# Kernel optimization log

Hardware: AMD Instinct MI355X
Metric: run time of the kernel (lower is better)

Reference implementation:

```python
import jax, jax.numpy as jnp
import numpy as np


def setup_inputs() -> dict:
    key = jax.random.key(0)
    k1, k2, k3 = jax.random.split(key, 3)
    N, M, H = 32768, 4096, 768
    fact = jax.random.normal(k1, (N, H), dtype=jnp.float32)
    elements_p = jax.random.normal(k2, (M, H), dtype=jnp.float32)
    # kaiming_uniform with a=sqrt(5) on [H,H]: bound = sqrt(6/((1+5)*H)) = 1/sqrt(H)
    bound = 1.0 / np.sqrt(H)
    weights = jax.random.uniform(k3, (H, H), dtype=jnp.float32, minval=-bound, maxval=bound)
    return {"fact": fact, "elements_p": elements_p, "weights": weights}


def reference(fact, elements_p, weights):
    # fact: [N,H], elements_p: [M,H], weights: [H,H]
    fact_Q = jnp.max(fact, axis=0, keepdims=True)                 # [1,H]
    f2e = (fact_Q @ weights) @ elements_p.T                        # [1,M]
    f2e = jax.nn.softmax(f2e, axis=-1)
    elements_p_ = jnp.sum(elements_p * f2e.T, axis=0, keepdims=True)  # [1,H]
    e2f = (fact @ weights) @ elements_p_.T                         # [N,1]
    e2f = jax.nn.softmax(e2f, axis=0)
    fact_ = jnp.sum(fact * e2f, axis=0, keepdims=True)             # [1,H]
    return (fact_, elements_p_)
```

## Files before the change

kernel.cpp:

```cpp
#include <hip/hip_runtime.h>
#include <math.h>


#define H 768
#define H4 192
#define PSTRIDE 772
#define ACC_OFF 4

__global__ __launch_bounds__(192) void k_colmax(const float4* __restrict__ x4,
                                                float4* __restrict__ pmax4, int N) {
  const int t = threadIdx.x;
  const int rpb = (N + gridDim.x - 1) / gridDim.x;
  const int n0 = blockIdx.x * rpb;
  const int n1 = min(N, n0 + rpb);
  float4 m = make_float4(-INFINITY, -INFINITY, -INFINITY, -INFINITY);
#pragma unroll 8
  for (int n = n0; n < n1; ++n) {
    float4 x = x4[(size_t)n * H4 + t];
    m.x = fmaxf(m.x, x.x); m.y = fmaxf(m.y, x.y);
    m.z = fmaxf(m.z, x.z); m.w = fmaxf(m.w, x.w);
  }
  pmax4[(size_t)blockIdx.x * H4 + t] = m;
}

__global__ __launch_bounds__(192) void k_q(const float4* __restrict__ W4,
                                           const float* __restrict__ pmax,
                                           float* __restrict__ q, int B) {
  const int tid = threadIdx.x;
  const int k0 = blockIdx.x * 16;
  __shared__ float sA[12][16];
  __shared__ float fQl[16];
  {
    const int col = tid & 15;
    const int grp = tid >> 4;
    float m = -INFINITY;
    for (int p = grp; p < B; p += 12) m = fmaxf(m, pmax[(size_t)p * H + k0 + col]);
    sA[grp][col] = m;
    __syncthreads();
    if (tid < 16) {
      float mm = sA[0][tid];
#pragma unroll
      for (int g = 1; g < 12; ++g) mm = fmaxf(mm, sA[g][tid]);
      fQl[tid] = mm;
    }
    __syncthreads();
  }
  float4 acc = make_float4(0.f, 0.f, 0.f, 0.f);
#pragma unroll 4
  for (int kk = 0; kk < 16; ++kk) {
    const float f = fQl[kk];
    const float4 w = W4[(size_t)(k0 + kk) * H4 + tid];
    acc.x = fmaf(f, w.x, acc.x);
    acc.y = fmaf(f, w.y, acc.y);
    acc.z = fmaf(f, w.z, acc.z);
    acc.w = fmaf(f, w.w, acc.w);
  }
  atomicAdd(&q[4 * tid + 0], acc.x);
  atomicAdd(&q[4 * tid + 1], acc.y);
  atomicAdd(&q[4 * tid + 2], acc.z);
  atomicAdd(&q[4 * tid + 3], acc.w);
}

template <int NW>
__global__ __launch_bounds__(NW * 64) void k_pass(const float4* __restrict__ X4,
                                                  const float* __restrict__ wvec,
                                                  float* __restrict__ part, int R,
                                                  unsigned int* __restrict__ cnt,
                                                  float* __restrict__ outA,
                                                  float* __restrict__ outB) {
  const int lane = threadIdx.x & 63;
  const int wv = threadIdx.x >> 6;
  const int NB = gridDim.x;
  __shared__ float sm[NW], sl[NW];
  __shared__ float4 sacc[NW][H4];

  {
    const int gw = blockIdx.x * NW + wv;
    const int nw = NB * NW;
    float4 wr[3];
#pragma unroll
    for (int j = 0; j < 3; ++j) wr[j] = ((const float4*)wvec)[lane + 64 * j];
    const int rpw = (R + nw - 1) / nw;
    const int r0 = gw * rpw;
    const int r1 = min(R, r0 + rpw);
    float mrun = -INFINITY, l = 0.f;
    float4 acc[3];
#pragma unroll
    for (int j = 0; j < 3; ++j) acc[j] = make_float4(0.f, 0.f, 0.f, 0.f);
    for (int r = r0; r < r1; ++r) {
      const float4* row = X4 + (size_t)r * H4;
      float4 x[3];
      float s = 0.f;
#pragma unroll
      for (int j = 0; j < 3; ++j) {
        x[j] = row[lane + 64 * j];
        s = fmaf(x[j].x, wr[j].x, s);
        s = fmaf(x[j].y, wr[j].y, s);
        s = fmaf(x[j].z, wr[j].z, s);
        s = fmaf(x[j].w, wr[j].w, s);
      }
#pragma unroll
      for (int o = 32; o; o >>= 1) s += __shfl_xor(s, o, 64);
      const float mn = fmaxf(mrun, s);
      const float esc = __expf(mrun - mn);
      const float p = __expf(s - mn);
      l = fmaf(l, esc, p);
#pragma unroll
      for (int j = 0; j < 3; ++j) {
        acc[j].x = fmaf(acc[j].x, esc, p * x[j].x);
        acc[j].y = fmaf(acc[j].y, esc, p * x[j].y);
        acc[j].z = fmaf(acc[j].z, esc, p * x[j].z);
        acc[j].w = fmaf(acc[j].w, esc, p * x[j].w);
      }
      mrun = mn;
    }
    if (lane == 0) { sm[wv] = mrun; sl[wv] = l; }
#pragma unroll
    for (int j = 0; j < 3; ++j) sacc[wv][lane + 64 * j] = acc[j];
    __syncthreads();
    if (wv == 0) {
      float gm = -INFINITY;
#pragma unroll
      for (int w2 = 0; w2 < NW; ++w2) gm = fmaxf(gm, sm[w2]);
      float fa[NW];
      float L = 0.f;
#pragma unroll
      for (int w2 = 0; w2 < NW; ++w2) {
        fa[w2] = (sl[w2] > 0.f) ? __expf(sm[w2] - gm) : 0.f;
        L = fmaf(fa[w2], sl[w2], L);
      }
      float* pb = part + (size_t)blockIdx.x * PSTRIDE;
#pragma unroll
      for (int j = 0; j < 3; ++j) {
        float4 a = make_float4(0.f, 0.f, 0.f, 0.f);
#pragma unroll
        for (int w2 = 0; w2 < NW; ++w2) {
          const float4 t = sacc[w2][lane + 64 * j];
          a.x = fmaf(fa[w2], t.x, a.x);
          a.y = fmaf(fa[w2], t.y, a.y);
          a.z = fmaf(fa[w2], t.z, a.z);
          a.w = fmaf(fa[w2], t.w, a.w);
        }
        *(float4*)(pb + ACC_OFF + 4 * (lane + 64 * j)) = a;
      }
      if (lane == 0) { pb[0] = gm; pb[1] = L; }
    }
  }

  __syncthreads();
  __shared__ unsigned int s_last;
  if (threadIdx.x == 0) {
    __threadfence();
    s_last = atomicAdd(cnt, 1u);
  }
  __syncthreads();
  if (s_last != (unsigned)(NB - 1)) return;
  __threadfence();

  {
    __shared__ float sred[NW];
    const float* P = part;
    float gm = -INFINITY;
    for (int b = threadIdx.x; b < NB; b += NW * 64) gm = fmaxf(gm, P[(size_t)b * PSTRIDE]);
#pragma unroll
    for (int o = 32; o; o >>= 1) gm = fmaxf(gm, __shfl_xor(gm, o, 64));
    if (lane == 0) sred[wv] = gm;
    __syncthreads();
    gm = sred[0];
#pragma unroll
    for (int w2 = 1; w2 < NW; ++w2) gm = fmaxf(gm, sred[w2]);
    __syncthreads();
    float L = 0.f;
    for (int b = threadIdx.x; b < NB; b += NW * 64) {
      const float m = P[(size_t)b * PSTRIDE];
      const float lb = P[(size_t)b * PSTRIDE + 1];
      L = fmaf((lb > 0.f) ? __expf(m - gm) : 0.f, lb, L);
    }
#pragma unroll
    for (int o = 32; o; o >>= 1) L += __shfl_xor(L, o, 64);
    if (lane == 0) sred[wv] = L;
    float4 a[3];
#pragma unroll
    for (int j = 0; j < 3; ++j) a[j] = make_float4(0.f, 0.f, 0.f, 0.f);
    for (int b = wv; b < NB; b += NW) {
      const float m = P[(size_t)b * PSTRIDE];
      const float lb = P[(size_t)b * PSTRIDE + 1];
      const float e = (lb > 0.f) ? __expf(m - gm) : 0.f;
      const float4* pa = (const float4*)(P + (size_t)b * PSTRIDE + ACC_OFF);
#pragma unroll
      for (int j = 0; j < 3; ++j) {
        const float4 t = pa[lane + 64 * j];
        a[j].x = fmaf(e, t.x, a[j].x);
        a[j].y = fmaf(e, t.y, a[j].y);
        a[j].z = fmaf(e, t.z, a[j].z);
        a[j].w = fmaf(e, t.w, a[j].w);
      }
    }
#pragma unroll
    for (int j = 0; j < 3; ++j) sacc[wv][lane + 64 * j] = a[j];
    __syncthreads();
    if (threadIdx.x < H4) {
      float4 s = sacc[0][threadIdx.x];
#pragma unroll
      for (int w2 = 1; w2 < NW; ++w2) {
        const float4 t = sacc[w2][threadIdx.x];
        s.x += t.x; s.y += t.y; s.z += t.z; s.w += t.w;
      }
      float Lt = sred[0];
#pragma unroll
      for (int w2 = 1; w2 < NW; ++w2) Lt += sred[w2];
      const float inv = 1.f / Lt;
      const float4 r = make_float4(s.x * inv, s.y * inv, s.z * inv, s.w * inv);
      ((float4*)outA)[threadIdx.x] = r;
      if (outB) ((float4*)outB)[threadIdx.x] = r;
    }
  }
}

__global__ __launch_bounds__(256) void k_v(const float4* __restrict__ W4,
                                           const float* __restrict__ ep_,
                                           float* __restrict__ v) {
  const int lane = threadIdx.x & 63;
  const int i = blockIdx.x * 4 + (threadIdx.x >> 6);
  float s = 0.f;
#pragma unroll
  for (int j = 0; j < 3; ++j) {
    const float4 w = W4[(size_t)i * H4 + lane + 64 * j];
    const float4 e = ((const float4*)ep_)[lane + 64 * j];
    s = fmaf(w.x, e.x, s);
    s = fmaf(w.y, e.y, s);
    s = fmaf(w.z, e.z, s);
    s = fmaf(w.w, e.w, s);
  }
#pragma unroll
  for (int o = 32; o; o >>= 1) s += __shfl_xor(s, o, 64);
  if (lane == 0) v[i] = s;
}

extern "C" void kernel_launch(void* const* d_in, const int* in_sizes, int n_in,
                              void* d_out, int out_size, void* d_ws, size_t ws_size,
                              hipStream_t stream) {
  const float* fact = (const float*)d_in[0];
  const float* ep   = (const float*)d_in[1];
  const float* W    = (const float*)d_in[2];
  float* out = (float*)d_out;
  const int N = in_sizes[0] / H;
  const int M = in_sizes[1] / H;

  const int B1 = 256;
  const int BM = 128;
  const int BN = 256;

  float* wsf  = (float*)d_ws;
  unsigned int* cnt2 = (unsigned int*)d_ws;
  unsigned int* cnt3 = (unsigned int*)d_ws + 1;
  float* q    = wsf + 4;
  float* epws = wsf + 772;
  float* v    = wsf + 1540;
  float* pmax = wsf + 2308;
  float* pm   = pmax + (size_t)B1 * H;
  float* pn   = pm + (size_t)BM * PSTRIDE;

  hipMemsetAsync(d_ws, 0, 3088, stream);
  k_colmax<<<B1, 192, 0, stream>>>((const float4*)fact, (float4*)pmax, N);
  k_q<<<48, 192, 0, stream>>>((const float4*)W, pmax, q, B1);
  k_pass<8><<<BM, 512, 0, stream>>>((const float4*)ep, q, pm, M, cnt2, epws, out + H);
  k_v<<<192, 256, 0, stream>>>((const float4*)W, epws, v);
  k_pass<8><<<BN, 512, 0, stream>>>((const float4*)fact, v, pn, N, cnt3, out, nullptr);
}
```

Baseline: 241.0 us.

## Fuse q projection, elements pass and v projection into one kernel; drop memset

Removes the memset by having the column-max kernel zero the counters, and fuses the q computation (global max reduce plus fQ@W) into the start of every elements-pass block. The last-arriving block then computes v = W·ep_ directly, which removes the separate k_q and k_v launches and their atomics. This cuts five launches plus a memset down to three kernels. The cost is that each of the 48 elements blocks redundantly reads all of W and the partial maxima. The elements pass also runs on fewer blocks, and the v matvec runs on a single block.

```diff
diff --git a/kernel.cpp b/kernel.cpp
--- a/kernel.cpp
+++ b/kernel.cpp
@@ -6,89 +6,102 @@
 #define H4 192
 #define PSTRIDE 772
 #define ACC_OFF 4
+#define B1 256
+#define B2 48
+#define B3 256
+
+__device__ __forceinline__ float wave_max(float x) {
+#pragma unroll
+  for (int o = 32; o; o >>= 1) x = fmaxf(x, __shfl_xor(x, o, 64));
+  return x;
+}
+__device__ __forceinline__ float wave_sum(float x) {
+#pragma unroll
+  for (int o = 32; o; o >>= 1) x += __shfl_xor(x, o, 64);
+  return x;
+}
+__device__ __forceinline__ float4 f4max(float4 a, float4 b) {
+  return make_float4(fmaxf(a.x, b.x), fmaxf(a.y, b.y), fmaxf(a.z, b.z), fmaxf(a.w, b.w));
+}
 
 __global__ __launch_bounds__(192) void k_colmax(const float4* __restrict__ x4,
-                                                float4* __restrict__ pmax4, int N) {
+                                                float4* __restrict__ pmax4, int N,
+                                                unsigned int* __restrict__ cnts) {
+  if (blockIdx.x == 0 && threadIdx.x < 2) cnts[threadIdx.x] = 0u;
   const int t = threadIdx.x;
-  const int rpb = (N + gridDim.x - 1) / gridDim.x;
+  const int rpb = (N + B1 - 1) / B1;
   const int n0 = blockIdx.x * rpb;
   const int n1 = min(N, n0 + rpb);
   float4 m = make_float4(-INFINITY, -INFINITY, -INFINITY, -INFINITY);
 #pragma unroll 8
-  for (int n = n0; n < n1; ++n) {
-    float4 x = x4[(size_t)n * H4 + t];
-    m.x = fmaxf(m.x, x.x); m.y = fmaxf(m.y, x.y);
-    m.z = fmaxf(m.z, x.z); m.w = fmaxf(m.w, x.w);
-  }
+  for (int n = n0; n < n1; ++n) m = f4max(m, x4[(size_t)n * H4 + t]);
   pmax4[(size_t)blockIdx.x * H4 + t] = m;
 }
 
-__global__ __launch_bounds__(192) void k_q(const float4* __restrict__ W4,
-                                           const float* __restrict__ pmax,
-                                           float* __restrict__ q, int B) {
+__global__ __launch_bounds__(512) void k_ep(const float4* __restrict__ ep4,
+                                            const float4* __restrict__ W4,
+                                            const float4* __restrict__ pmax4,
+                                            float* __restrict__ part, int M,
+                                            unsigned int* __restrict__ cnt,
+                                            float* __restrict__ out_ep,
+                                            float* __restrict__ v) {
   const int tid = threadIdx.x;
-  const int k0 = blockIdx.x * 16;
-  __shared__ float sA[12][16];
-  __shared__ float fQl[16];
+  const int lane = tid & 63;
+  const int wv = tid >> 6;
+  __shared__ float4 sacc[8][H4];
+  __shared__ float4 fq4[H4];
+  __shared__ float4 qarr4[H4];
+  __shared__ float sred[16];
+  __shared__ float se[B2];
+  __shared__ unsigned int s_last;
+
+  if (tid < 2 * H4) {
+    const int g = tid / H4, c = tid % H4;
+    float4 m = make_float4(-INFINITY, -INFINITY, -INFINITY, -INFINITY);
+#pragma unroll 8
+    for (int p = g; p < B1; p += 2) m = f4max(m, pmax4[(size_t)p * H4 + c]);
+    ((float4*)sacc)[g * H4 + c] = m;
+  }
+  __syncthreads();
+  if (tid < H4) fq4[tid] = f4max(((float4*)sacc)[tid], ((float4*)sacc)[H4 + tid]);
+  __syncthreads();
+  if (tid < 2 * H4) {
+    const int g = tid / H4, c = tid % H4;
+    const float* fq = (const float*)fq4;
+    float4 a = make_float4(0.f, 0.f, 0.f, 0.f);
+#pragma unroll 4
+    for (int k = g * 384; k < g * 384 + 384; ++k) {
+      const float f = fq[k];
+      const float4 w = W4[(size_t)k * H4 + c];
+      a.x = fmaf(f, w.x, a.x);
+      a.y = fmaf(f, w.y, a.y);
+      a.z = fmaf(f, w.z, a.z);
+      a.w = fmaf(f, w.w, a.w);
+    }
+    ((float4*)sacc)[g * H4 + c] = a;
+  }
+  __syncthreads();
+  if (tid < H4) {
+    const float4 a = ((float4*)sacc)[tid], b = ((float4*)sacc)[H4 + tid];
+    qarr4[tid] = make_float4(a.x + b.x, a.y + b.y, a.z + b.z, a.w + b.w);
+  }
+  __syncthreads();
+
   {
-    const int col = tid & 15;
-    const int grp = tid >> 4;
-    float m = -INFINITY;
-    for (int p = grp; p < B; p += 12) m = fmaxf(m, pmax[(size_t)p * H + k0 + col]);
-    sA[grp][col] = m;
-    __syncthreads();
-    if (tid < 16) {
-      float mm = sA[0][tid];
-#pragma unroll
-      for (int g = 1; g < 12; ++g) mm = fmaxf(mm, sA[g][tid]);
-      fQl[tid] = mm;
-    }
-    __syncthreads();
-  }
-  float4 acc = make_float4(0.f, 0.f, 0.f, 0.f);
-#pragma unroll 4
-  for (int kk = 0; kk < 16; ++kk) {
-    const float f = fQl[kk];
-    const float4 w = W4[(size_t)(k0 + kk) * H4 + tid];
-    acc.x = fmaf(f, w.x, acc.x);
-    acc.y = fmaf(f, w.y, acc.y);
-    acc.z = fmaf(f, w.z, acc.z);
-    acc.w = fmaf(f, w.w, acc.w);
-  }
-  atomicAdd(&q[4 * tid + 0], acc.x);
-  atomicAdd(&q[4 * tid + 1], acc.y);
-  atomicAdd(&q[4 * tid + 2], acc.z);
-  atomicAdd(&q[4 * tid + 3], acc.w);
-}
-
-template <int NW>
-__global__ __launch_bounds__(NW * 64) void k_pass(const float4* __restrict__ X4,
-                                                  const float* __restrict__ wvec,
-                                                  float* __restrict__ part, int R,
-                                                  unsigned int* __restrict__ cnt,
-                                                  float* __restrict__ outA,
-                                                  float* __restrict__ outB) {
-  const int lane = threadIdx.x & 63;
-  const int wv = threadIdx.x >> 6;
-  const int NB = gridDim.x;
-  __shared__ float sm[NW], sl[NW];
-  __shared__ float4 sacc[NW][H4];
-
-  {
-    const int gw = blockIdx.x * NW + wv;
-    const int nw = NB * NW;
     float4 wr[3];
 #pragma unroll
-    for (int j = 0; j < 3; ++j) wr[j] = ((const float4*)wvec)[lane + 64 * j];
-    const int rpw = (R + nw - 1) / nw;
+    for (int j = 0; j < 3; ++j) wr[j] = qarr4[lane + 64 * j];
+    const int nw = B2 * 8;
+    const int gw = blockIdx.x * 8 + wv;
+    const int rpw = (M + nw - 1) / nw;
     const int r0 = gw * rpw;
-    const int r1 = min(R, r0 + rpw);
+    const int r1 = min(M, r0 + rpw);
     float mrun = -INFINITY, l = 0.f;
     float4 acc[3];
 #pragma unroll
     for (int j = 0; j < 3; ++j) acc[j] = make_float4(0.f, 0.f, 0.f, 0.f);
     for (int r = r0; r < r1; ++r) {
-      const float4* row = X4 + (size_t)r * H4;
+      const float4* row = ep4 + (size_t)r * H4;
       float4 x[3];
       float s = 0.f;
 #pragma unroll
@@ -99,8 +112,7 @@
         s = fmaf(x[j].z, wr[j].z, s);
         s = fmaf(x[j].w, wr[j].w, s);
       }
-#pragma unroll
-      for (int o = 32; o; o >>= 1) s += __shfl_xor(s, o, 64);
+      s = wave_sum(s);
       const float mn = fmaxf(mrun, s);
       const float esc = __expf(mrun - mn);
       const float p = __expf(s - mn);
@@ -114,27 +126,28 @@
       }
       mrun = mn;
     }
-    if (lane == 0) { sm[wv] = mrun; sl[wv] = l; }
+    if (lane == 0) { sred[wv] = mrun; sred[8 + wv] = l; }
 #pragma unroll
     for (int j = 0; j < 3; ++j) sacc[wv][lane + 64 * j] = acc[j];
     __syncthreads();
     if (wv == 0) {
       float gm = -INFINITY;
 #pragma unroll
-      for (int w2 = 0; w2 < NW; ++w2) gm = fmaxf(gm, sm[w2]);
-      float fa[NW];
+      for (int w2 = 0; w2 < 8; ++w2) gm = fmaxf(gm, sred[w2]);
+      float fa[8];
       float L = 0.f;
 #pragma unroll
-      for (int w2 = 0; w2 < NW; ++w2) {
-        fa[w2] = (sl[w2] > 0.f) ? __expf(sm[w2] - gm) : 0.f;
-        L = fmaf(fa[w2], sl[w2], L);
+      for (int w2 = 0; w2 < 8; ++w2) {
+        const float lw = sred[8 + w2];
+        fa[w2] = (lw > 0.f) ? __expf(sred[w2] - gm) : 0.f;
+        L = fmaf(fa[w2], lw, L);
       }
       float* pb = part + (size_t)blockIdx.x * PSTRIDE;
 #pragma unroll
       for (int j = 0; j < 3; ++j) {
         float4 a = make_float4(0.f, 0.f, 0.f, 0.f);
 #pragma unroll
-        for (int w2 = 0; w2 < NW; ++w2) {
+        for (int w2 = 0; w2 < 8; ++w2) {
           const float4 t = sacc[w2][lane + 64 * j];
           a.x = fmaf(fa[w2], t.x, a.x);
           a.y = fmaf(fa[w2], t.y, a.y);
@@ -148,41 +161,205 @@
   }
 
   __syncthreads();
-  __shared__ unsigned int s_last;
-  if (threadIdx.x == 0) {
+  if (tid == 0) {
     __threadfence();
     s_last = atomicAdd(cnt, 1u);
   }
   __syncthreads();
-  if (s_last != (unsigned)(NB - 1)) return;
+  if (s_last != (unsigned)(B2 - 1)) return;
   __threadfence();
 
   {
-    __shared__ float sred[NW];
     const float* P = part;
     float gm = -INFINITY;
-    for (int b = threadIdx.x; b < NB; b += NW * 64) gm = fmaxf(gm, P[(size_t)b * PSTRIDE]);
-#pragma unroll
-    for (int o = 32; o; o >>= 1) gm = fmaxf(gm, __shfl_xor(gm, o, 64));
+    for (int b = tid; b < B2; b += 512) gm = fmaxf(gm, P[(size_t)b * PSTRIDE]);
+    gm = wave_max(gm);
     if (lane == 0) sred[wv] = gm;
     __syncthreads();
     gm = sred[0];
 #pragma unroll
-    for (int w2 = 1; w2 < NW; ++w2) gm = fmaxf(gm, sred[w2]);
-    __syncthreads();
+    for (int w2 = 1; w2 < 8; ++w2) gm = fmaxf(gm, sred[w2]);
     float L = 0.f;
-    for (int b = threadIdx.x; b < NB; b += NW * 64) {
+    for (int b = tid; b < B2; b += 512) {
+      const float m = P[(size_t)b * PSTRIDE];
+      const float lb = P[(size_t)b * PSTRIDE + 1];
+      const float e = (lb > 0.f) ? __expf(m - gm) : 0.f;
+      se[b] = e;
+      L = fmaf(e, lb, L);
+    }
+    L = wave_sum(L);
+    if (lane == 0) sred[8 + wv] = L;
+    __syncthreads();
+    float Lt = sred[8];
+#pragma unroll
+    for (int w2 = 1; w2 < 8; ++w2) Lt += sred[8 + w2];
+    if (tid < H4) {
+      float4 a = make_float4(0.f, 0.f, 0.f, 0.f);
+#pragma unroll 4
+      for (int b = 0; b < B2; ++b) {
+        const float e = se[b];
+        const float4 t = *(const float4*)(P + (size_t)b * PSTRIDE + ACC_OFF + 4 * tid);
+        a.x = fmaf(e, t.x, a.x);
+        a.y = fmaf(e, t.y, a.y);
+        a.z = fmaf(e, t.z, a.z);
+        a.w = fmaf(e, t.w, a.w);
+      }
+      const float inv = 1.f / Lt;
+      const float4 r = make_float4(a.x * inv, a.y * inv, a.z * inv, a.w * inv);
+      ((float4*)out_ep)[tid] = r;
+      fq4[tid] = r;
+    }
+    __syncthreads();
+    float4 er[3];
+#pragma unroll
+    for (int j = 0; j < 3; ++j) er[j] = fq4[lane + 64 * j];
+    for (int i0 = wv * 96; i0 < wv * 96 + 96; i0 += 4) {
+      float s0 = 0.f, s1 = 0.f, s2 = 0.f, s3 = 0.f;
+#pragma unroll
+      for (int j = 0; j < 3; ++j) {
+        const float4 e = er[j];
+        const float4 w0 = W4[(size_t)(i0 + 0) * H4 + lane + 64 * j];
+        const float4 w1 = W4[(size_t)(i0 + 1) * H4 + lane + 64 * j];
+        const float4 w2 = W4[(size_t)(i0 + 2) * H4 + lane + 64 * j];
+        const float4 w3 = W4[(size_t)(i0 + 3) * H4 + lane + 64 * j];
+        s0 = fmaf(w0.x, e.x, s0); s0 = fmaf(w0.y, e.y, s0);
+        s0 = fmaf(w0.z, e.z, s0); s0 = fmaf(w0.w, e.w, s0);
+        s1 = fmaf(w1.x, e.x, s1); s1 = fmaf(w1.y, e.y, s1);
+        s1 = fmaf(w1.z, e.z, s1); s1 = fmaf(w1.w, e.w, s1);
+        s2 = fmaf(w2.x, e.x, s2); s2 = fmaf(w2.y, e.y, s2);
+        s2 = fmaf(w2.z, e.z, s2); s2 = fmaf(w2.w, e.w, s2);
+        s3 = fmaf(w3.x, e.x, s3); s3 = fmaf(w3.y, e.y, s3);
+        s3 = fmaf(w3.z, e.z, s3); s3 = fmaf(w3.w, e.w, s3);
+      }
+#pragma unroll
+      for (int o = 32; o; o >>= 1) {
+        s0 += __shfl_xor(s0, o, 64);
+        s1 += __shfl_xor(s1, o, 64);
+        s2 += __shfl_xor(s2, o, 64);
+        s3 += __shfl_xor(s3, o, 64);
+      }
+      if (lane == 0) ((float4*)v)[i0 >> 2] = make_float4(s0, s1, s2, s3);
+    }
+  }
+}
+
+__global__ __launch_bounds__(512) void k_fact(const float4* __restrict__ X4,
+                                              const float* __restrict__ wvec,
+                                              float* __restrict__ part, int R,
+                                              unsigned int* __restrict__ cnt,
+                                              float* __restrict__ outp) {
+  const int tid = threadIdx.x;
+  const int lane = tid & 63;
+  const int wv = tid >> 6;
+  __shared__ float sm[8], sl[8];
+  __shared__ float4 sacc[8][H4];
+  __shared__ unsigned int s_last;
+
+  {
+    float4 wr[3];
+#pragma unroll
+    for (int j = 0; j < 3; ++j) wr[j] = ((const float4*)wvec)[lane + 64 * j];
+    const int nw = B3 * 8;
+    const int gw = blockIdx.x * 8 + wv;
+    const int rpw = (R + nw - 1) / nw;
+    const int r0 = gw * rpw;
+    const int r1 = min(R, r0 + rpw);
+    float mrun = -INFINITY, l = 0.f;
+    float4 acc[3];
+#pragma unroll
+    for (int j = 0; j < 3; ++j) acc[j] = make_float4(0.f, 0.f, 0.f, 0.f);
+    for (int r = r0; r < r1; ++r) {
+      const float4* row = X4 + (size_t)r * H4;
+      float4 x[3];
+      float s = 0.f;
+#pragma unroll
+      for (int j = 0; j < 3; ++j) {
+        x[j] = row[lane + 64 * j];
+        s = fmaf(x[j].x, wr[j].x, s);
+        s = fmaf(x[j].y, wr[j].y, s);
+        s = fmaf(x[j].z, wr[j].z, s);
+        s = fmaf(x[j].w, wr[j].w, s);
+      }
+      s = wave_sum(s);
+      const float mn = fmaxf(mrun, s);
+      const float esc = __expf(mrun - mn);
+      const float p = __expf(s - mn);
+      l = fmaf(l, esc, p);
+#pragma unroll
+      for (int j = 0; j < 3; ++j) {
+        acc[j].x = fmaf(acc[j].x, esc, p * x[j].x);
+        acc[j].y = fmaf(acc[j].y, esc, p * x[j].y);
+        acc[j].z = fmaf(acc[j].z, esc, p * x[j].z);
+        acc[j].w = fmaf(acc[j].w, esc, p * x[j].w);
+      }
+      mrun = mn;
+    }
+    if (lane == 0) { sm[wv] = mrun; sl[wv] = l; }
+#pragma unroll
+    for (int j = 0; j < 3; ++j) sacc[wv][lane + 64 * j] = acc[j];
+    __syncthreads();
+    if (wv == 0) {
+      float gm = -INFINITY;
+#pragma unroll
+      for (int w2 = 0; w2 < 8; ++w2) gm = fmaxf(gm, sm[w2]);
+      float fa[8];
+      float L = 0.f;
+#pragma unroll
+      for (int w2 = 0; w2 < 8; ++w2) {
+        fa[w2] = (sl[w2] > 0.f) ? __expf(sm[w2] - gm) : 0.f;
+        L = fmaf(fa[w2], sl[w2], L);
+      }
+      float* pb = part + (size_t)blockIdx.x * PSTRIDE;
+#pragma unroll
+      for (int j = 0; j < 3; ++j) {
+        float4 a = make_float4(0.f, 0.f, 0.f, 0.f);
+#pragma unroll
+        for (int w2 = 0; w2 < 8; ++w2) {
+          const float4 t = sacc[w2][lane + 64 * j];
+          a.x = fmaf(fa[w2], t.x, a.x);
+          a.y = fmaf(fa[w2], t.y, a.y);
+          a.z = fmaf(fa[w2], t.z, a.z);
+          a.w = fmaf(fa[w2], t.w, a.w);
+        }
+        *(float4*)(pb + ACC_OFF + 4 * (lane + 64 * j)) = a;
+      }
+      if (lane == 0) { pb[0] = gm; pb[1] = L; }
+    }
+  }
+
+  __syncthreads();
+  if (tid == 0) {
+    __threadfence();
+    s_last = atomicAdd(cnt, 1u);
+  }
+  __syncthreads();
+  if (s_last != (unsigned)(B3 - 1)) return;
+  __threadfence();
+
+  {
+    __shared__ float sred[16];
+    const float* P = part;
+    float gm = -INFINITY;
+    for (int b = tid; b < B3; b += 512) gm = fmaxf(gm, P[(size_t)b * PSTRIDE]);
+    gm = wave_max(gm);
+    if (lane == 0) sred[wv] = gm;
+    __syncthreads();
+    gm = sred[0];
+#pragma unroll
+    for (int w2 = 1; w2 < 8; ++w2) gm = fmaxf(gm, sred[w2]);
+    __syncthreads();
+    float L = 0.f;
+    for (int b = tid; b < B3; b += 512) {
       const float m = P[(size_t)b * PSTRIDE];
       const float lb = P[(size_t)b * PSTRIDE + 1];
       L = fmaf((lb > 0.f) ? __expf(m - gm) : 0.f, lb, L);
     }
-#pragma unroll
-    for (int o = 32; o; o >>= 1) L += __shfl_xor(L, o, 64);
-    if (lane == 0) sred[wv] = L;
+    L = wave_sum(L);
+    if (lane == 0) sred[8 + wv] = L;
     float4 a[3];
 #pragma unroll
     for (int j = 0; j < 3; ++j) a[j] = make_float4(0.f, 0.f, 0.f, 0.f);
-    for (int b = wv; b < NB; b += NW) {
+    for (int b = wv; b < B3; b += 8) {
       const float m = P[(size_t)b * PSTRIDE];
       const float lb = P[(size_t)b * PSTRIDE + 1];
       const float e = (lb > 0.f) ? __expf(m - gm) : 0.f;
@@ -199,72 +376,40 @@
 #pragma unroll
     for (int j = 0; j < 3; ++j) sacc[wv][lane + 64 * j] = a[j];
     __syncthreads();
-    if (threadIdx.x < H4) {
-      float4 s = sacc[0][threadIdx.x];
-#pragma unroll
-      for (int w2 = 1; w2 < NW; ++w2) {
-        const float4 t = sacc[w2][threadIdx.x];
+    if (tid < H4) {
+      float4 s = sacc[0][tid];
+#pragma unroll
+      for (int w2 = 1; w2 < 8; ++w2) {
+        const float4 t = sacc[w2][tid];
         s.x += t.x; s.y += t.y; s.z += t.z; s.w += t.w;
       }
-      float Lt = sred[0];
-#pragma unroll
-      for (int w2 = 1; w2 < NW; ++w2) Lt += sred[w2];
+      float Lt = sred[8];
+#pragma unroll
+      for (int w2 = 1; w2 < 8; ++w2) Lt += sred[8 + w2];
       const float inv = 1.f / Lt;
-      const float4 r = make_float4(s.x * inv, s.y * inv, s.z * inv, s.w * inv);
-      ((float4*)outA)[threadIdx.x] = r;
-      if (outB) ((float4*)outB)[threadIdx.x] = r;
-    }
-  }
-}
-
-__global__ __launch_bounds__(256) void k_v(const float4* __restrict__ W4,
-                                           const float* __restrict__ ep_,
-                                           float* __restrict__ v) {
-  const int lane = threadIdx.x & 63;
-  const int i = blockIdx.x * 4 + (threadIdx.x >> 6);
-  float s = 0.f;
-#pragma unroll
-  for (int j = 0; j < 3; ++j) {
-    const float4 w = W4[(size_t)i * H4 + lane + 64 * j];
-    const float4 e = ((const float4*)ep_)[lane + 64 * j];
-    s = fmaf(w.x, e.x, s);
-    s = fmaf(w.y, e.y, s);
-    s = fmaf(w.z, e.z, s);
-    s = fmaf(w.w, e.w, s);
-  }
-#pragma unroll
-  for (int o = 32; o; o >>= 1) s += __shfl_xor(s, o, 64);
-  if (lane == 0) v[i] = s;
+      ((float4*)outp)[tid] = make_float4(s.x * inv, s.y * inv, s.z * inv, s.w * inv);
+    }
+  }
 }
 
 extern "C" void kernel_launch(void* const* d_in, const int* in_sizes, int n_in,
                               void* d_out, int out_size, void* d_ws, size_t ws_size,
                               hipStream_t stream) {
-  const float* fact = (const float*)d_in[0];
-  const float* ep   = (const float*)d_in[1];
-  const float* W    = (const float*)d_in[2];
+  const float4* fact4 = (const float4*)d_in[0];
+  const float4* ep4   = (const float4*)d_in[1];
+  const float4* W4    = (const float4*)d_in[2];
   float* out = (float*)d_out;
   const int N = in_sizes[0] / H;
   const int M = in_sizes[1] / H;
 
-  const int B1 = 256;
-  const int BM = 128;
-  const int BN = 256;
-
-  float* wsf  = (float*)d_ws;
-  unsigned int* cnt2 = (unsigned int*)d_ws;
-  unsigned int* cnt3 = (unsigned int*)d_ws + 1;
-  float* q    = wsf + 4;
-  float* epws = wsf + 772;
-  float* v    = wsf + 1540;
-  float* pmax = wsf + 2308;
-  float* pm   = pmax + (size_t)B1 * H;
-  float* pn   = pm + (size_t)BM * PSTRIDE;
-
-  hipMemsetAsync(d_ws, 0, 3088, stream);
-  k_colmax<<<B1, 192, 0, stream>>>((const float4*)fact, (float4*)pmax, N);
-  k_q<<<48, 192, 0, stream>>>((const float4*)W, pmax, q, B1);
-  k_pass<8><<<BM, 512, 0, stream>>>((const float4*)ep, q, pm, M, cnt2, epws, out + H);
-  k_v<<<192, 256, 0, stream>>>((const float4*)W, epws, v);
-  k_pass<8><<<BN, 512, 0, stream>>>((const float4*)fact, v, pn, N, cnt3, out, nullptr);
-}
+  float* wsf = (float*)d_ws;
+  unsigned int* cnts = (unsigned int*)d_ws;
+  float* v = wsf + 4;
+  float4* pmax4 = (float4*)(wsf + 4 + H);
+  float* pm = wsf + 4 + H + B1 * H;
+  float* pn = pm + (size_t)B2 * PSTRIDE;
+
+  k_colmax<<<B1, 192, 0, stream>>>(fact4, pmax4, N, cnts);
+  k_ep<<<B2, 512, 0, stream>>>(ep4, W4, pmax4, pm, M, cnts + 0, out + H, v);
+  k_fact<<<B3, 512, 0, stream>>>(fact4, v, pn, N, cnts + 1, out);
+}
```

Measured after the change: 307.0 us. 27.4% more time.

## Fuse W·ep_ matvec into last block of ep pass and drop memset launch

Applied to the files above, without the earlier changes.

Removes the hipMemsetAsync by zeroing counters and q inside block 0 of the colmax kernel. Folds the separate k_v matvec into the last-arriving block of the elements pass, which computes v from the combined ep_ held in LDS. Also raises the elements-pass grid from 128 to 256 blocks. Together these cut two launches, but the W·ep_ product (768x768) now runs serially on a single block after the grid-wide combine. The memset-to-colmax move also relies on kernel ordering: k_q's atomics must not start before block 0 has zeroed q.

```diff
diff --git a/kernel.cpp b/kernel.cpp
--- a/kernel.cpp
+++ b/kernel.cpp
@@ -6,20 +6,186 @@
 #define H4 192
 #define PSTRIDE 772
 #define ACC_OFF 4
+#define B1 256
+#define BQ 48
+#define B2 256
+#define B3 256
+
+__device__ __forceinline__ float wave_max(float x) {
+#pragma unroll
+  for (int o = 32; o; o >>= 1) x = fmaxf(x, __shfl_xor(x, o, 64));
+  return x;
+}
+__device__ __forceinline__ float wave_sum(float x) {
+#pragma unroll
+  for (int o = 32; o; o >>= 1) x += __shfl_xor(x, o, 64);
+  return x;
+}
+__device__ __forceinline__ float4 f4max(float4 a, float4 b) {
+  return make_float4(fmaxf(a.x, b.x), fmaxf(a.y, b.y), fmaxf(a.z, b.z), fmaxf(a.w, b.w));
+}
+
+struct SMem {
+  float4 sacc[8][H4];
+  float sred[16];
+  float4 sep[H4];
+};
+
+__device__ __forceinline__ void stream_pass(const float4* __restrict__ X4,
+                                            const float* __restrict__ wvec,
+                                            float* __restrict__ part, int R,
+                                            int NBk, SMem& sm) {
+  const int tid = threadIdx.x;
+  const int lane = tid & 63;
+  const int wv = tid >> 6;
+  float4 wr[3];
+#pragma unroll
+  for (int j = 0; j < 3; ++j) wr[j] = ((const float4*)wvec)[lane + 64 * j];
+  const int nw = NBk * 8;
+  const int gw = blockIdx.x * 8 + wv;
+  const int rpw = (R + nw - 1) / nw;
+  const int r0 = gw * rpw;
+  const int r1 = min(R, r0 + rpw);
+  float mrun = -INFINITY, l = 0.f;
+  float4 acc[3];
+#pragma unroll
+  for (int j = 0; j < 3; ++j) acc[j] = make_float4(0.f, 0.f, 0.f, 0.f);
+  for (int r = r0; r < r1; ++r) {
+    const float4* row = X4 + (size_t)r * H4;
+    float4 x[3];
+    float s = 0.f;
+#pragma unroll
+    for (int j = 0; j < 3; ++j) {
+      x[j] = row[lane + 64 * j];
+      s = fmaf(x[j].x, wr[j].x, s);
+      s = fmaf(x[j].y, wr[j].y, s);
+      s = fmaf(x[j].z, wr[j].z, s);
+      s = fmaf(x[j].w, wr[j].w, s);
+    }
+    s = wave_sum(s);
+    const float mn = fmaxf(mrun, s);
+    const float esc = __expf(mrun - mn);
+    const float p = __expf(s - mn);
+    l = fmaf(l, esc, p);
+#pragma unroll
+    for (int j = 0; j < 3; ++j) {
+      acc[j].x = fmaf(acc[j].x, esc, p * x[j].x);
+      acc[j].y = fmaf(acc[j].y, esc, p * x[j].y);
+      acc[j].z = fmaf(acc[j].z, esc, p * x[j].z);
+      acc[j].w = fmaf(acc[j].w, esc, p * x[j].w);
+    }
+    mrun = mn;
+  }
+  if (lane == 0) { sm.sred[wv] = mrun; sm.sred[8 + wv] = l; }
+#pragma unroll
+  for (int j = 0; j < 3; ++j) sm.sacc[wv][lane + 64 * j] = acc[j];
+  __syncthreads();
+  if (wv == 0) {
+    float gm = -INFINITY;
+#pragma unroll
+    for (int w2 = 0; w2 < 8; ++w2) gm = fmaxf(gm, sm.sred[w2]);
+    float fa[8];
+    float L = 0.f;
+#pragma unroll
+    for (int w2 = 0; w2 < 8; ++w2) {
+      const float lw = sm.sred[8 + w2];
+      fa[w2] = (lw > 0.f) ? __expf(sm.sred[w2] - gm) : 0.f;
+      L = fmaf(fa[w2], lw, L);
+    }
+    float* pb = part + (size_t)blockIdx.x * PSTRIDE;
+#pragma unroll
+    for (int j = 0; j < 3; ++j) {
+      float4 a = make_float4(0.f, 0.f, 0.f, 0.f);
+#pragma unroll
+      for (int w2 = 0; w2 < 8; ++w2) {
+        const float4 t = sm.sacc[w2][lane + 64 * j];
+        a.x = fmaf(fa[w2], t.x, a.x);
+        a.y = fmaf(fa[w2], t.y, a.y);
+        a.z = fmaf(fa[w2], t.z, a.z);
+        a.w = fmaf(fa[w2], t.w, a.w);
+      }
+      *(float4*)(pb + ACC_OFF + 4 * (lane + 64 * j)) = a;
+    }
+    if (lane == 0) { pb[0] = gm; pb[1] = L; }
+  }
+}
+
+__device__ __forceinline__ void combine_all(const float* __restrict__ P, int NBk,
+                                            float* __restrict__ dst, bool keep_lds,
+                                            SMem& sm) {
+  const int tid = threadIdx.x;
+  const int lane = tid & 63;
+  const int wv = tid >> 6;
+  float gm = -INFINITY;
+  for (int b = tid; b < NBk; b += 512) gm = fmaxf(gm, P[(size_t)b * PSTRIDE]);
+  gm = wave_max(gm);
+  if (lane == 0) sm.sred[wv] = gm;
+  __syncthreads();
+  gm = sm.sred[0];
+#pragma unroll
+  for (int w2 = 1; w2 < 8; ++w2) gm = fmaxf(gm, sm.sred[w2]);
+  __syncthreads();
+  float L = 0.f;
+  for (int b = tid; b < NBk; b += 512) {
+    const float m = P[(size_t)b * PSTRIDE];
+    const float lb = P[(size_t)b * PSTRIDE + 1];
+    L = fmaf((lb > 0.f) ? __expf(m - gm) : 0.f, lb, L);
+  }
+  L = wave_sum(L);
+  if (lane == 0) sm.sred[8 + wv] = L;
+  float4 a[3];
+#pragma unroll
+  for (int j = 0; j < 3; ++j) a[j] = make_float4(0.f, 0.f, 0.f, 0.f);
+  for (int b = wv; b < NBk; b += 8) {
+    const float m = P[(size_t)b * PSTRIDE];
+    const float lb = P[(size_t)b * PSTRIDE + 1];
+    const float e = (lb > 0.f) ? __expf(m - gm) : 0.f;
+    const float4* pa = (const float4*)(P + (size_t)b * PSTRIDE + ACC_OFF);
+#pragma unroll
+    for (int j = 0; j < 3; ++j) {
+      const float4 t = pa[lane + 64 * j];
+      a[j].x = fmaf(e, t.x, a[j].x);
+      a[j].y = fmaf(e, t.y, a[j].y);
+      a[j].z = fmaf(e, t.z, a[j].z);
+      a[j].w = fmaf(e, t.w, a[j].w);
+    }
+  }
+#pragma unroll
+  for (int j = 0; j < 3; ++j) sm.sacc[wv][lane + 64 * j] = a[j];
+  __syncthreads();
+  if (tid < H4) {
+    float4 s = sm.sacc[0][tid];
+#pragma unroll
+    for (int w2 = 1; w2 < 8; ++w2) {
+      const float4 t = sm.sacc[w2][tid];
+      s.x += t.x; s.y += t.y; s.z += t.z; s.w += t.w;
+    }
+    float Lt = sm.sred[8];
+#pragma unroll
+    for (int w2 = 1; w2 < 8; ++w2) Lt += sm.sred[8 + w2];
+    const float inv = 1.f / Lt;
+    const float4 r = make_float4(s.x * inv, s.y * inv, s.z * inv, s.w * inv);
+    ((float4*)dst)[tid] = r;
+    if (keep_lds) sm.sep[tid] = r;
+  }
+}
 
 __global__ __launch_bounds__(192) void k_colmax(const float4* __restrict__ x4,
-                                                float4* __restrict__ pmax4, int N) {
+                                                float4* __restrict__ pmax4, int N,
+                                                unsigned int* __restrict__ cnts,
+                                                float* __restrict__ q) {
   const int t = threadIdx.x;
-  const int rpb = (N + gridDim.x - 1) / gridDim.x;
+  if (blockIdx.x == 0) {
+    if (t < 2) cnts[t] = 0u;
+#pragma unroll
+    for (int j = 0; j < 4; ++j) q[t + 192 * j] = 0.f;
+  }
+  const int rpb = (N + B1 - 1) / B1;
   const int n0 = blockIdx.x * rpb;
   const int n1 = min(N, n0 + rpb);
   float4 m = make_float4(-INFINITY, -INFINITY, -INFINITY, -INFINITY);
 #pragma unroll 8
-  for (int n = n0; n < n1; ++n) {
-    float4 x = x4[(size_t)n * H4 + t];
-    m.x = fmaxf(m.x, x.x); m.y = fmaxf(m.y, x.y);
-    m.z = fmaxf(m.z, x.z); m.w = fmaxf(m.w, x.w);
-  }
+  for (int n = n0; n < n1; ++n) m = f4max(m, x4[(size_t)n * H4 + t]);
   pmax4[(size_t)blockIdx.x * H4 + t] = m;
 }
 
@@ -61,210 +227,108 @@
   atomicAdd(&q[4 * tid + 3], acc.w);
 }
 
-template <int NW>
-__global__ __launch_bounds__(NW * 64) void k_pass(const float4* __restrict__ X4,
-                                                  const float* __restrict__ wvec,
-                                                  float* __restrict__ part, int R,
-                                                  unsigned int* __restrict__ cnt,
-                                                  float* __restrict__ outA,
-                                                  float* __restrict__ outB) {
-  const int lane = threadIdx.x & 63;
-  const int wv = threadIdx.x >> 6;
-  const int NB = gridDim.x;
-  __shared__ float sm[NW], sl[NW];
-  __shared__ float4 sacc[NW][H4];
-
-  {
-    const int gw = blockIdx.x * NW + wv;
-    const int nw = NB * NW;
-    float4 wr[3];
-#pragma unroll
-    for (int j = 0; j < 3; ++j) wr[j] = ((const float4*)wvec)[lane + 64 * j];
-    const int rpw = (R + nw - 1) / nw;
-    const int r0 = gw * rpw;
-    const int r1 = min(R, r0 + rpw);
-    float mrun = -INFINITY, l = 0.f;
-    float4 acc[3];
-#pragma unroll
-    for (int j = 0; j < 3; ++j) acc[j] = make_float4(0.f, 0.f, 0.f, 0.f);
-    for (int r = r0; r < r1; ++r) {
-      const float4* row = X4 + (size_t)r * H4;
-      float4 x[3];
-      float s = 0.f;
-#pragma unroll
-      for (int j = 0; j < 3; ++j) {
-        x[j] = row[lane + 64 * j];
-        s = fmaf(x[j].x, wr[j].x, s);
-        s = fmaf(x[j].y, wr[j].y, s);
-        s = fmaf(x[j].z, wr[j].z, s);
-        s = fmaf(x[j].w, wr[j].w, s);
-      }
-#pragma unroll
-      for (int o = 32; o; o >>= 1) s += __shfl_xor(s, o, 64);
-      const float mn = fmaxf(mrun, s);
-      const float esc = __expf(mrun - mn);
-      const float p = __expf(s - mn);
-      l = fmaf(l, esc, p);
-#pragma unroll
-      for (int j = 0; j < 3; ++j) {
-        acc[j].x = fmaf(acc[j].x, esc, p * x[j].x);
-        acc[j].y = fmaf(acc[j].y, esc, p * x[j].y);
-        acc[j].z = fmaf(acc[j].z, esc, p * x[j].z);
-        acc[j].w = fmaf(acc[j].w, esc, p * x[j].w);
-      }
-      mrun = mn;
-    }
-    if (lane == 0) { sm[wv] = mrun; sl[wv] = l; }
-#pragma unroll
-    for (int j = 0; j < 3; ++j) sacc[wv][lane + 64 * j] = acc[j];
-    __syncthreads();
-    if (wv == 0) {
-      float gm = -INFINITY;
-#pragma unroll
-      for (int w2 = 0; w2 < NW; ++w2) gm = fmaxf(gm, sm[w2]);
-      float fa[NW];
-      float L = 0.f;
-#pragma unroll
-      for (int w2 = 0; w2 < NW; ++w2) {
-        fa[w2] = (sl[w2] > 0.f) ? __expf(sm[w2] - gm) : 0.f;
-        L = fmaf(fa[w2], sl[w2], L);
-      }
-      float* pb = part + (size_t)blockIdx.x * PSTRIDE;
-#pragma unroll
-      for (int j = 0; j < 3; ++j) {
-        float4 a = make_float4(0.f, 0.f, 0.f, 0.f);
-#pragma unroll
-        for (int w2 = 0; w2 < NW; ++w2) {
-          const float4 t = sacc[w2][lane + 64 * j];
-          a.x = fmaf(fa[w2], t.x, a.x);
-          a.y = fmaf(fa[w2], t.y, a.y);
-          a.z = fmaf(fa[w2], t.z, a.z);
-          a.w = fmaf(fa[w2], t.w, a.w);
-        }
-        *(float4*)(pb + ACC_OFF + 4 * (lane + 64 * j)) = a;
-      }
-      if (lane == 0) { pb[0] = gm; pb[1] = L; }
-    }
-  }
-
-  __syncthreads();
+__global__ __launch_bounds__(512) void k_ep(const float4* __restrict__ ep4,
+                                            const float4* __restrict__ W4,
+                                            const float* __restrict__ q,
+                                            float* __restrict__ part, int M,
+                                            unsigned int* __restrict__ cnt,
+                                            float* __restrict__ out_ep,
+                                            float* __restrict__ v) {
+  const int tid = threadIdx.x;
+  const int lane = tid & 63;
+  const int wv = tid >> 6;
+  __shared__ SMem sm;
   __shared__ unsigned int s_last;
-  if (threadIdx.x == 0) {
+
+  stream_pass(ep4, q, part, M, B2, sm);
+
+  __syncthreads();
+  if (tid == 0) {
     __threadfence();
     s_last = atomicAdd(cnt, 1u);
   }
   __syncthreads();
-  if (s_last != (unsigned)(NB - 1)) return;
+  if (s_last != (unsigned)(B2 - 1)) return;
   __threadfence();
 
-  {
-    __shared__ float sred[NW];
-    const float* P = part;
-    float gm = -INFINITY;
-    for (int b = threadIdx.x; b < NB; b += NW * 64) gm = fmaxf(gm, P[(size_t)b * PSTRIDE]);
-#pragma unroll
-    for (int o = 32; o; o >>= 1) gm = fmaxf(gm, __shfl_xor(gm, o, 64));
-    if (lane == 0) sred[wv] = gm;
-    __syncthreads();
-    gm = sred[0];
-#pragma unroll
-    for (int w2 = 1; w2 < NW; ++w2) gm = fmaxf(gm, sred[w2]);
-    __syncthreads();
-    float L = 0.f;
-    for (int b = threadIdx.x; b < NB; b += NW * 64) {
-      const float m = P[(size_t)b * PSTRIDE];
-      const float lb = P[(size_t)b * PSTRIDE + 1];
-      L = fmaf((lb > 0.f) ? __expf(m - gm) : 0.f, lb, L);
-    }
-#pragma unroll
-    for (int o = 32; o; o >>= 1) L += __shfl_xor(L, o, 64);
-    if (lane == 0) sred[wv] = L;
-    float4 a[3];
-#pragma unroll
-    for (int j = 0; j < 3; ++j) a[j] = make_float4(0.f, 0.f, 0.f, 0.f);
-    for (int b = wv; b < NB; b += NW) {
-      const float m = P[(size_t)b * PSTRIDE];
-      const float lb = P[(size_t)b * PSTRIDE + 1];
-      const float e = (lb > 0.f) ? __expf(m - gm) : 0.f;
-      const float4* pa = (const float4*)(P + (size_t)b * PSTRIDE + ACC_OFF);
-#pragma unroll
-      for (int j = 0; j < 3; ++j) {
-        const float4 t = pa[lane + 64 * j];
-        a[j].x = fmaf(e, t.x, a[j].x);
-        a[j].y = fmaf(e, t.y, a[j].y);
-        a[j].z = fmaf(e, t.z, a[j].z);
-        a[j].w = fmaf(e, t.w, a[j].w);
-      }
-    }
-#pragma unroll
-    for (int j = 0; j < 3; ++j) sacc[wv][lane + 64 * j] = a[j];
-    __syncthreads();
-    if (threadIdx.x < H4) {
-      float4 s = sacc[0][threadIdx.x];
-#pragma unroll
-      for (int w2 = 1; w2 < NW; ++w2) {
-        const float4 t = sacc[w2][threadIdx.x];
-        s.x += t.x; s.y += t.y; s.z += t.z; s.w += t.w;
-      }
-      float Lt = sred[0];
-#pragma unroll
-      for (int w2 = 1; w2 < NW; ++w2) Lt += sred[w2];
-      const float inv = 1.f / Lt;
-      const float4 r = make_float4(s.x * inv, s.y * inv, s.z * inv, s.w * inv);
-      ((float4*)outA)[threadIdx.x] = r;
-      if (outB) ((float4*)outB)[threadIdx.x] = r;
-    }
-  }
-}
-
-__global__ __launch_bounds__(256) void k_v(const float4* __restrict__ W4,
-                                           const float* __restrict__ ep_,
-                                           float* __restrict__ v) {
-  const int lane = threadIdx.x & 63;
-  const int i = blockIdx.x * 4 + (threadIdx.x >> 6);
-  float s = 0.f;
-#pragma unroll
-  for (int j = 0; j < 3; ++j) {
-    const float4 w = W4[(size_t)i * H4 + lane + 64 * j];
-    const float4 e = ((const float4*)ep_)[lane + 64 * j];
-    s = fmaf(w.x, e.x, s);
-    s = fmaf(w.y, e.y, s);
-    s = fmaf(w.z, e.z, s);
-    s = fmaf(w.w, e.w, s);
-  }
-#pragma unroll
-  for (int o = 32; o; o >>= 1) s += __shfl_xor(s, o, 64);
-  if (lane == 0) v[i] = s;
+  combine_all(part, B2, out_ep, true, sm);
+  __syncthreads();
+
+  float4 er[3];
+#pragma unroll
+  for (int j = 0; j < 3; ++j) er[j] = sm.sep[lane + 64 * j];
+  for (int i0 = wv * 96; i0 < wv * 96 + 96; i0 += 4) {
+    float s0 = 0.f, s1 = 0.f, s2 = 0.f, s3 = 0.f;
+#pragma unroll
+    for (int j = 0; j < 3; ++j) {
+      const float4 e = er[j];
+      const float4 w0 = W4[(size_t)(i0 + 0) * H4 + lane + 64 * j];
+      const float4 w1 = W4[(size_t)(i0 + 1) * H4 + lane + 64 * j];
+      const float4 w2 = W4[(size_t)(i0 + 2) * H4 + lane + 64 * j];
+      const float4 w3 = W4[(size_t)(i0 + 3) * H4 + lane + 64 * j];
+      s0 = fmaf(w0.x, e.x, s0); s0 = fmaf(w0.y, e.y, s0);
+      s0 = fmaf(w0.z, e.z, s0); s0 = fmaf(w0.w, e.w, s0);
+      s1 = fmaf(w1.x, e.x, s1); s1 = fmaf(w1.y, e.y, s1);
+      s1 = fmaf(w1.z, e.z, s1); s1 = fmaf(w1.w, e.w, s1);
+      s2 = fmaf(w2.x, e.x, s2); s2 = fmaf(w2.y, e.y, s2);
+      s2 = fmaf(w2.z, e.z, s2); s2 = fmaf(w2.w, e.w, s2);
+      s3 = fmaf(w3.x, e.x, s3); s3 = fmaf(w3.y, e.y, s3);
+      s3 = fmaf(w3.z, e.z, s3); s3 = fmaf(w3.w, e.w, s3);
+    }
+#pragma unroll
+    for (int o = 32; o; o >>= 1) {
+      s0 += __shfl_xor(s0, o, 64);
+      s1 += __shfl_xor(s1, o, 64);
+      s2 += __shfl_xor(s2, o, 64);
+      s3 += __shfl_xor(s3, o, 64);
+    }
+    if (lane == 0) ((float4*)v)[i0 >> 2] = make_float4(s0, s1, s2, s3);
+  }
+}
+
+__global__ __launch_bounds__(512) void k_fact(const float4* __restrict__ X4,
+                                              const float* __restrict__ v,
+                                              float* __restrict__ part, int R,
+                                              unsigned int* __restrict__ cnt,
+                                              float* __restrict__ outp) {
+  const int tid = threadIdx.x;
+  __shared__ SMem sm;
+  __shared__ unsigned int s_last;
+
+  stream_pass(X4, v, part, R, B3, sm);
+
+  __syncthreads();
+  if (tid == 0) {
+    __threadfence();
+    s_last = atomicAdd(cnt, 1u);
+  }
+  __syncthreads();
+  if (s_last != (unsigned)(B3 - 1)) return;
+  __threadfence();
+
+  combine_all(part, B3, outp, false, sm);
 }
 
 extern "C" void kernel_launch(void* const* d_in, const int* in_sizes, int n_in,
                               void* d_out, int out_size, void* d_ws, size_t ws_size,
                               hipStream_t stream) {
-  const float* fact = (const float*)d_in[0];
-  const float* ep   = (const float*)d_in[1];
-  const float* W    = (const float*)d_in[2];
+  const float4* fact4 = (const float4*)d_in[0];
+  const float4* ep4   = (const float4*)d_in[1];
+  const float4* W4    = (const float4*)d_in[2];
   float* out = (float*)d_out;
   const int N = in_sizes[0] / H;
   const int M = in_sizes[1] / H;
 
-  const int B1 = 256;
-  const int BM = 128;
-  const int BN = 256;
-
-  float* wsf  = (float*)d_ws;
-  unsigned int* cnt2 = (unsigned int*)d_ws;
-  unsigned int* cnt3 = (unsigned int*)d_ws + 1;
-  float* q    = wsf + 4;
-  float* epws = wsf + 772;
-  float* v    = wsf + 1540;
-  float* pmax = wsf + 2308;
-  float* pm   = pmax + (size_t)B1 * H;
-  float* pn   = pm + (size_t)BM * PSTRIDE;
-
-  hipMemsetAsync(d_ws, 0, 3088, stream);
-  k_colmax<<<B1, 192, 0, stream>>>((const float4*)fact, (float4*)pmax, N);
-  k_q<<<48, 192, 0, stream>>>((const float4*)W, pmax, q, B1);
-  k_pass<8><<<BM, 512, 0, stream>>>((const float4*)ep, q, pm, M, cnt2, epws, out + H);
-  k_v<<<192, 256, 0, stream>>>((const float4*)W, epws, v);
-  k_pass<8><<<BN, 512, 0, stream>>>((const float4*)fact, v, pn, N, cnt3, out, nullptr);
-}
+  float* wsf = (float*)d_ws;
+  unsigned int* cnts = (unsigned int*)d_ws;
+  float* q = wsf + 4;
+  float* v = wsf + 4 + H;
+  float* pmaxf = wsf + 4 + 2 * H;
+  float* pm = pmaxf + (size_t)B1 * H;
+  float* pn = pm + (size_t)B2 * PSTRIDE;
+
+  k_colmax<<<B1, 192, 0, stream>>>(fact4, (float4*)pmaxf, N, cnts, q);
+  k_q<<<BQ, 192, 0, stream>>>(W4, pmaxf, q, B1);
+  k_ep<<<B2, 512, 0, stream>>>(ep4, W4, q, pm, M, cnts + 0, out + H, v);
+  k_fact<<<B3, 512, 0, stream>>>(fact4, v, pn, N, cnts + 1, out);
+}
```

Measured after the change: 285.1 us. 18.3% more time.
